# Kernel optimization log

Measured on AMD Instinct MI355X. Metric: run time of the kernel, lower is better.

## Reference

```python
import jax, jax.numpy as jnp
import numpy as np
from jax import lax

A_NUM = 2
N_LAYER = 4
DIM0 = 64   # fr_inner_dim_0 == signal_dim_0 (forced by view/squeeze logic)
DIM1 = 256  # fr_inner_dim_1
SD0 = 64
SD1 = 64
K_OUT = 8
UPS = 4
EPS = 1e-5
BSZ = 64


def setup_inputs() -> dict:
    key = jax.random.key(0)
    ks = jax.random.split(key, 16)
    s = 0.05
    f32 = jnp.float32
    inp = jax.random.normal(ks[0], (BSZ, 2, SD0, SD1), f32)
    # ComplexConv2d2 weights stored squeezed to their effective matmul form.
    W_in_r = jax.random.normal(ks[1], (DIM1 * A_NUM, SD1), f32) * s
    W_in_i = jax.random.normal(ks[2], (DIM1 * A_NUM, SD1), f32) * s
    W_pre_r = jax.random.normal(ks[3], (A_NUM,), f32) * s
    W_pre_i = jax.random.normal(ks[4], (A_NUM,), f32) * s
    Wm_r = jax.random.normal(ks[5], (2 * N_LAYER, SD0, SD0), f32) * s
    Wm_i = jax.random.normal(ks[6], (2 * N_LAYER, SD0, SD0), f32) * s
    Wc_r = jax.random.normal(ks[7], (N_LAYER, A_NUM), f32) * s
    Wc_i = jax.random.normal(ks[8], (N_LAYER, A_NUM), f32) * s
    W_l3_r = jax.random.normal(ks[9], (DIM0 * A_NUM, SD0), f32) * s
    W_l3_i = jax.random.normal(ks[10], (DIM0 * A_NUM, SD0), f32) * s
    conv1_w = jax.random.normal(ks[11], (N_LAYER, A_NUM, A_NUM, 3, 3), f32) * s
    conv2_w = jax.random.normal(ks[12], (N_LAYER, A_NUM, A_NUM, 3, 3), f32) * s
    bn1_g = jnp.ones((N_LAYER, A_NUM), f32)
    bn1_b = jnp.zeros((N_LAYER, A_NUM), f32)
    bn2_g = jnp.ones((N_LAYER, A_NUM), f32)
    bn2_b = jnp.zeros((N_LAYER, A_NUM), f32)
    W_out = jax.random.normal(ks[13], (A_NUM, 1, K_OUT, K_OUT), f32) * s
    return {"inp": inp, "W_in_r": W_in_r, "W_in_i": W_in_i, "W_pre_r": W_pre_r,
            "W_pre_i": W_pre_i, "Wm_r": Wm_r, "Wm_i": Wm_i, "Wc_r": Wc_r,
            "Wc_i": Wc_i, "W_l3_r": W_l3_r, "W_l3_i": W_l3_i,
            "conv1_w": conv1_w, "bn1_g": bn1_g, "bn1_b": bn1_b,
            "conv2_w": conv2_w, "bn2_g": bn2_g, "bn2_b": bn2_b, "W_out": W_out}


def _circ_conv(x, w):
    xp = jnp.pad(x, ((0, 0), (0, 0), (1, 1), (1, 1)), mode='wrap')
    return lax.conv_general_dilated(xp, w, (1, 1), 'VALID',
                                    dimension_numbers=('NCHW', 'OIHW', 'NCHW'))


def _bn(x, g, b):
    mu = jnp.mean(x, axis=(0, 2, 3), keepdims=True)
    var = jnp.var(x, axis=(0, 2, 3), keepdims=True)
    return (x - mu) * lax.rsqrt(var + EPS) * g[None, :, None, None] + b[None, :, None, None]


def _forward(inp, W_in_r, W_in_i, W_pre_r, W_pre_i, Wm_r, Wm_i, Wc_r, Wc_i,
             W_l3_r, W_l3_i, conv1_w, bn1_g, bn1_b, conv2_w, bn2_g, bn2_b, W_out):
    bsz = inp.shape[0]
    xr, xi = inp[:, 0], inp[:, 1]  # (b, sd0, sd1)
    # input_layer: complex conv, kernel (1, sd1) -> contraction over width
    yr = jnp.einsum('bhw,cw->bch', xr, W_in_r) - jnp.einsum('bhw,cw->bch', xi, W_in_i)
    yi = jnp.einsum('bhw,cw->bch', xi, W_in_r) + jnp.einsum('bhw,cw->bch', xr, W_in_i)
    xreal = yr.reshape(bsz, A_NUM, DIM1, DIM0).transpose(0, 1, 3, 2)  # (b,A,dim0,dim1)
    ximag = yi.reshape(bsz, A_NUM, DIM1, DIM0).transpose(0, 1, 3, 2)
    # concat_pre: complex 1x1 conv, A_NUM -> 1 channel
    x_real = (jnp.einsum('bahw,a->bhw', xreal, W_pre_r) - jnp.einsum('bahw,a->bhw', ximag, W_pre_i))[:, None]
    x_imag = (jnp.einsum('bahw,a->bhw', ximag, W_pre_r) + jnp.einsum('bahw,a->bhw', xreal, W_pre_i))[:, None]
    Gr, Gi = x_real, x_imag  # loop-invariant Gnk

    def phase_branch(xr_, xi_, Wr, Wi):
        a, c = xr_[:, 0], xi_[:, 0]  # (b, dim0, dim1)
        # complex conv kernel (sd0,1) == matmul over height
        Ir = (jnp.einsum('bhw,ch->bcw', a, Wr) - jnp.einsum('bhw,ch->bcw', c, Wi))[:, None]
        Ii = (jnp.einsum('bhw,ch->bcw', c, Wr) + jnp.einsum('bhw,ch->bcw', a, Wi))[:, None]
        s_ = 1.0 + jnp.log(Ir * Ir + Ii * Ii)
        EIr, EIi = s_ * Ir, -s_ * Ii
        ur, ui = Wr.T, Wi.T
        zr = jnp.einsum('hc,bncw->bnhw', ur, EIr) - jnp.einsum('hc,bncw->bnhw', ui, EIi)
        zi = jnp.einsum('hc,bncw->bnhw', ur, EIi) + jnp.einsum('hc,bncw->bnhw', ui, EIr)
        wr = jnp.sum(Gr * zr - Gi * zi, axis=3)  # (b,1,dim0)
        wi = jnp.sum(Gr * zi + Gi * zr, axis=3)
        ang = jnp.arctan2(wi, wr)[..., None]  # broadcast over dim1
        cr, ci = jnp.cos(ang), -jnp.sin(ang)
        return Gr * cr - Gi * ci, Gr * ci + Gi * cr

    for i in range(N_LAYER):
        x1r, x1i = phase_branch(x_real, x_imag, Wm_r[i], Wm_i[i])
        x2r, x2i = phase_branch(x_real, x_imag, Wm_r[i + N_LAYER], Wm_i[i + N_LAYER])
        sr = jnp.concatenate([x1r, x2r], 1)
        si = jnp.concatenate([x1i, x2i], 1)
        x_real = (jnp.einsum('bahw,a->bhw', sr, Wc_r[i]) - jnp.einsum('bahw,a->bhw', si, Wc_i[i]))[:, None]
        x_imag = (jnp.einsum('bahw,a->bhw', si, Wc_r[i]) + jnp.einsum('bahw,a->bhw', sr, Wc_i[i]))[:, None]

    # input_layer3: complex conv kernel (sd0,1), 1 -> dim0*A_NUM channels
    a, c = x_real[:, 0], x_imag[:, 0]
    fr = (jnp.einsum('bhw,ch->bcw', a, W_l3_r) - jnp.einsum('bhw,ch->bcw', c, W_l3_i)).reshape(bsz, -1)
    fi = (jnp.einsum('bhw,ch->bcw', c, W_l3_r) + jnp.einsum('bhw,ch->bcw', a, W_l3_i)).reshape(bsz, -1)
    m = jnp.max(jnp.sqrt(fr * fr + fi * fi), axis=1, keepdims=True)
    fr, fi = fr / m, fi / m
    fr = fr.reshape(bsz, A_NUM, DIM0, DIM1)
    fi = fi.reshape(bsz, A_NUM, DIM0, DIM1)
    x = jnp.sqrt(fr * fr + fi * fi)

    for i in range(N_LAYER):
        h = jax.nn.relu(_bn(_circ_conv(x, conv1_w[i]), bn1_g[i], bn1_b[i]))
        h = _bn(_circ_conv(h, conv2_w[i]), bn2_g[i], bn2_b[i])
        x = jax.nn.relu(x + h)

    # ConvTranspose2d(A_NUM, 1, K_OUT, stride=UPS, padding=2, output_padding=1)
    wt = jnp.flip(W_out, (2, 3)).transpose(1, 0, 2, 3)  # (1, A_NUM, k, k)
    pad_lo = K_OUT - 1 - 2
    pad_hi = pad_lo + 1
    y = lax.conv_general_dilated(x, wt, (1, 1),
                                 [(pad_lo, pad_hi), (pad_lo, pad_hi)],
                                 lhs_dilation=(UPS, UPS),
                                 dimension_numbers=('NCHW', 'OIHW', 'NCHW'))
    return y[:, 0]


def reference(inp, W_in_r, W_in_i, W_pre_r, W_pre_i, Wm_r, Wm_i, Wc_r, Wc_i,
              W_l3_r, W_l3_i, conv1_w, bn1_g, bn1_b, conv2_w, bn2_g, bn2_b, W_out):
    return _forward(inp, W_in_r, W_in_i, W_pre_r, W_pre_i, Wm_r, Wm_i, Wc_r, Wc_i,
                    W_l3_r, W_l3_i, conv1_w, bn1_g, bn1_b, conv2_w, bn2_g, bn2_b, W_out)
```

## Files before the change

### kernel.cpp

```cpp
#include <hip/hip_runtime.h>
#include <hip/hip_bf16.h>
#include <math.h>


__global__ void k0_prep(const float* __restrict__ Wr, const float* __restrict__ Wi,
                        const float* __restrict__ pr, const float* __restrict__ pi,
                        float* __restrict__ ArT, float* __restrict__ AiT,
                        float2* __restrict__ C) {
    int w  = blockIdx.x;
    int w2 = threadIdx.x;
    float p0r = pr[0], p1r = pr[1], p0i = pi[0], p1i = pi[1];
    float wr0 = Wr[w2 * 64 + w],         wi0 = Wi[w2 * 64 + w];
    float wr1 = Wr[(256 + w2) * 64 + w], wi1 = Wi[(256 + w2) * 64 + w];
    ArT[w * 256 + w2] = p0r * wr0 - p0i * wi0 + p1r * wr1 - p1i * wi1;
    AiT[w * 256 + w2] = p0r * wi0 + p0i * wr0 + p1r * wi1 + p1i * wr1;
    if (w2 < 64) C[w * 64 + w2] = make_float2(1.f, 0.f);
}

__global__ void k0b_T(const float* __restrict__ Wmr, const float* __restrict__ Wmi,
                      float* __restrict__ WmrT, float* __restrict__ WmiT) {
    int m = blockIdx.x;
    int t = threadIdx.x;
    const float* sr = Wmr + m * 4096;
    const float* si = Wmi + m * 4096;
    float* dr = WmrT + m * 4096;
    float* di = WmiT + m * 4096;
    for (int k = t; k < 4096; k += 256) {
        int c = k >> 6, h = k & 63;
        dr[h * 64 + c] = sr[k];
        di[h * 64 + c] = si[k];
    }
}

__global__ __launch_bounds__(256) void k1_G(const float* __restrict__ inp,
                                            const float* __restrict__ ArT,
                                            const float* __restrict__ AiT,
                                            float* __restrict__ Gr, float* __restrict__ Gi) {
    int hc = blockIdx.x;
    int b  = blockIdx.y;
    int t  = threadIdx.x;
    __shared__ float sxr[8][64], sxi[8][64];
    int base_r = (b * 2 + 0) * 4096 + hc * 8 * 64;
    int base_i = (b * 2 + 1) * 4096 + hc * 8 * 64;
    for (int k = t; k < 512; k += 256) {
        int r = k >> 6, w = k & 63;
        sxr[r][w] = inp[base_r + r * 64 + w];
        sxi[r][w] = inp[base_i + r * 64 + w];
    }
    __syncthreads();
    float accr[8], acci[8];
#pragma unroll
    for (int r = 0; r < 8; r++) { accr[r] = 0.f; acci[r] = 0.f; }
    for (int k = 0; k < 64; k++) {
        float ar = ArT[k * 256 + t], ai = AiT[k * 256 + t];
#pragma unroll
        for (int r = 0; r < 8; r++) {
            float xr = sxr[r][k], xi = sxi[r][k];
            accr[r] += xr * ar - xi * ai;
            acci[r] += xi * ar + xr * ai;
        }
    }
#pragma unroll
    for (int r = 0; r < 8; r++) {
        int h = hc * 8 + r;
        Gr[(b * 64 + h) * 256 + t] = accr[r];
        Gi[(b * 64 + h) * 256 + t] = acci[r];
    }
}

__global__ __launch_bounds__(512) void k2_layer(const float* __restrict__ Gr,
                                                const float* __restrict__ Gi,
                                                const float2* __restrict__ C,
                                                const float* __restrict__ Wmr,
                                                const float* __restrict__ Wmi,
                                                const float* __restrict__ WmrT,
                                                const float* __restrict__ WmiT,
                                                float2* __restrict__ wsum, int layer) {
    int wc = blockIdx.x;
    int b  = blockIdx.y;
    int t = threadIdx.x, tx = t & 63, ty = t >> 6;
    __shared__ float2 sX[4096];
    __shared__ float2 sE[4096];
    int h0 = __builtin_amdgcn_readfirstlane(ty << 3);

    int gbase = b * 16384 + wc * 64 + tx;
    float gr_[8], gi_[8];
#pragma unroll
    for (int r = 0; r < 8; r++) {
        int h = h0 + r;
        float gr = Gr[gbase + h * 256], gi = Gi[gbase + h * 256];
        gr_[r] = gr; gi_[r] = gi;
        float2 c = C[b * 64 + h];
        sX[h * 64 + tx] = make_float2(c.x * gr - c.y * gi, c.x * gi + c.y * gr);
    }
    __syncthreads();

    for (int j = 0; j < 2; j++) {
        int mat = layer + 4 * j;
        const float* Wr0  = Wmr  + mat * 4096 + h0 * 64;
        const float* Wi0  = Wmi  + mat * 4096 + h0 * 64;
        const float* WrT0 = WmrT + mat * 4096 + h0 * 64;
        const float* WiT0 = WmiT + mat * 4096 + h0 * 64;

        float Ir[8] = {0,0,0,0,0,0,0,0}, Ii[8] = {0,0,0,0,0,0,0,0};
#pragma unroll 4
        for (int h = 0; h < 64; h++) {
            float2 x = sX[h * 64 + tx];
#pragma unroll
            for (int r = 0; r < 8; r++) {
                float wr = Wr0[r * 64 + h], wi = Wi0[r * 64 + h];
                Ir[r] += wr * x.x - wi * x.y;
                Ii[r] += wr * x.y + wi * x.x;
            }
        }
#pragma unroll
        for (int r = 0; r < 8; r++) {
            float m2 = Ir[r] * Ir[r] + Ii[r] * Ii[r];
            float s = 1.f + __logf(m2);
            sE[(h0 + r) * 64 + tx] = make_float2(s * Ir[r], -s * Ii[r]);
        }
        __syncthreads();

        float Zr[8] = {0,0,0,0,0,0,0,0}, Zi[8] = {0,0,0,0,0,0,0,0};
#pragma unroll 4
        for (int c = 0; c < 64; c++) {
            float2 e = sE[c * 64 + tx];
#pragma unroll
            for (int r = 0; r < 8; r++) {
                float wr = WrT0[r * 64 + c], wi = WiT0[r * 64 + c];
                Zr[r] += wr * e.x - wi * e.y;
                Zi[r] += wr * e.y + wi * e.x;
            }
        }
#pragma unroll
        for (int r = 0; r < 8; r++) {
            int h = h0 + r;
            float pr = gr_[r] * Zr[r] - gi_[r] * Zi[r];
            float pi = gr_[r] * Zi[r] + gi_[r] * Zr[r];
#pragma unroll
            for (int off = 32; off > 0; off >>= 1) {
                pr += __shfl_xor(pr, off);
                pi += __shfl_xor(pi, off);
            }
            if (tx == 0) wsum[((b * 64 + h) * 2 + j) * 4 + wc] = make_float2(pr, pi);
        }
        __syncthreads();
    }
}

__global__ void k3_cupdate(const float2* __restrict__ wsum, float2* __restrict__ C,
                           const float* __restrict__ Wcr, const float* __restrict__ Wci,
                           int layer) {
    int id = blockIdx.x * 256 + threadIdx.x;
    float accr = 0.f, acci = 0.f;
#pragma unroll
    for (int j = 0; j < 2; j++) {
        float wr = 0.f, wi = 0.f;
#pragma unroll
        for (int wc = 0; wc < 4; wc++) {
            float2 p = wsum[(id * 2 + j) * 4 + wc];
            wr += p.x; wi += p.y;
        }
        float m2 = wr * wr + wi * wi;
        float cr, ci;
        if (m2 > 0.f) {
            float inv = 1.f / sqrtf(m2);
            cr = wr * inv; ci = -wi * inv;
        } else { cr = 1.f; ci = 0.f; }
        float wcr = Wcr[layer * 2 + j], wci = Wci[layer * 2 + j];
        accr += cr * wcr - ci * wci;
        acci += ci * wcr + cr * wci;
    }
    C[id] = make_float2(accr, acci);
}

__global__ __launch_bounds__(1024) void k4_proj(const float* __restrict__ Gr,
                                                const float* __restrict__ Gi,
                                                const float2* __restrict__ C,
                                                const float* __restrict__ W3r,
                                                const float* __restrict__ W3i,
                                                float* __restrict__ xmag,
                                                float* __restrict__ pmax) {
    int wc = blockIdx.x;
    int cb = blockIdx.y;
    int b  = blockIdx.z;
    int t = threadIdx.x, tx = t & 63, ty = t >> 6;
    __shared__ float2 sX[4096];
    int c0 = __builtin_amdgcn_readfirstlane(ty << 2);
    const float* W3r0 = W3r + (cb * 64 + c0) * 64;
    const float* W3i0 = W3i + (cb * 64 + c0) * 64;
    int gbase = b * 16384 + wc * 64 + tx;
#pragma unroll
    for (int r = 0; r < 4; r++) {
        int h = (ty << 2) + r;
        float gr = Gr[gbase + h * 256], gi = Gi[gbase + h * 256];
        float2 c = C[b * 64 + h];
        sX[h * 64 + tx] = make_float2(c.x * gr - c.y * gi, c.x * gi + c.y * gr);
    }
    __syncthreads();
    float Fr[4] = {0,0,0,0}, Fi[4] = {0,0,0,0};
#pragma unroll 8
    for (int h = 0; h < 64; h++) {
        float2 x = sX[h * 64 + tx];
#pragma unroll
        for (int r = 0; r < 4; r++) {
            float wr = W3r0[r * 64 + h], wi = W3i0[r * 64 + h];
            Fr[r] += wr * x.x - wi * x.y;
            Fi[r] += wr * x.y + wi * x.x;
        }
    }
    float mx = 0.f;
#pragma unroll
    for (int r = 0; r < 4; r++) {
        int cl = (ty << 2) + r;
        float mag = sqrtf(Fr[r] * Fr[r] + Fi[r] * Fi[r]);
        xmag[(b * 128 + cb * 64 + cl) * 256 + wc * 64 + tx] = mag;
        mx = fmaxf(mx, mag);
    }
#pragma unroll
    for (int off = 32; off > 0; off >>= 1) mx = fmaxf(mx, __shfl_xor(mx, off));
    __syncthreads();
    float* scratch = (float*)sX;
    if (tx == 0) scratch[ty] = mx;
    __syncthreads();
    if (t == 0) {
        float m = scratch[0];
#pragma unroll
        for (int k = 1; k < 16; k++) m = fmaxf(m, scratch[k]);
        pmax[b * 8 + cb * 4 + wc] = m;
    }
}

__global__ __launch_bounds__(256) void k_conv1f(const float* __restrict__ xin,
                                                const float* __restrict__ h2,
                                                const float* __restrict__ cw,
                                                const float* __restrict__ stats2,
                                                const float* __restrict__ pmax,
                                                float* __restrict__ hout,
                                                float* __restrict__ xout,
                                                float* __restrict__ psum,
                                                float* __restrict__ psumsq,
                                                int layer) {
    int hb = blockIdx.x;
    int co = blockIdx.y;
    int b  = blockIdx.z;
    int tx = threadIdx.x;
    float wgt[18];
    const float* wp = cw + layer * 36 + co * 18;
#pragma unroll
    for (int k = 0; k < 18; k++) wgt[k] = wp[k];
    float sc0 = 0.f, sc1 = 0.f, sh0 = 0.f, sh1 = 0.f, inv = 1.f;
    if (layer == 0) {
        float m = 0.f;
#pragma unroll
        for (int k = 0; k < 8; k++) m = fmaxf(m, pmax[b * 8 + k]);
        inv = 1.f / m;
    } else {
        sc0 = stats2[0]; sc1 = stats2[1]; sh0 = stats2[2]; sh1 = stats2[3];
    }
    int wm = (tx + 255) & 255, wpp = (tx + 1) & 255;
    float lsum = 0.f, lsq = 0.f;
    for (int r = 0; r < 4; r++) {
        int hh = hb * 4 + r;
        int hm = (hh + 63) & 63, hp = (hh + 1) & 63;
        const int rows[3] = {hm, hh, hp};
        const int cols[3] = {wm, tx, wpp};
        float acc = 0.f;
#pragma unroll
        for (int ci = 0; ci < 2; ci++) {
            const float* xp  = xin + (b * 2 + ci) * 16384;
            const float* hp2 = h2  + (b * 2 + ci) * 16384;
            float sc = ci ? sc1 : sc0, sh = ci ? sh1 : sh0;
            const float* wg = wgt + ci * 9;
#pragma unroll
            for (int kh = 0; kh < 3; kh++)
#pragma unroll
                for (int kw = 0; kw < 3; kw++) {
                    int idx = rows[kh] * 256 + cols[kw];
                    float v;
                    if (layer == 0) v = xp[idx] * inv;
                    else            v = fmaxf(xp[idx] + hp2[idx] * sc + sh, 0.f);
                    if (ci == co && kh == 1 && kw == 1)
                        xout[(b * 2 + co) * 16384 + hh * 256 + tx] = v;
                    acc += wg[kh * 3 + kw] * v;
                }
        }
        hout[((b * 2 + co) * 64 + hh) * 256 + tx] = acc;
        lsum += acc; lsq += acc * acc;
    }
#pragma unroll
    for (int off = 32; off > 0; off >>= 1) {
        lsum += __shfl_xor(lsum, off);
        lsq  += __shfl_xor(lsq, off);
    }
    __shared__ float ssum[4], ssq[4];
    int tyy = tx >> 6, lane = tx & 63;
    if (lane == 0) { ssum[tyy] = lsum; ssq[tyy] = lsq; }
    __syncthreads();
    if (tx == 0) {
        int bl = b * 16 + hb;
        psum[co * 1024 + bl]   = ssum[0] + ssum[1] + ssum[2] + ssum[3];
        psumsq[co * 1024 + bl] = ssq[0] + ssq[1] + ssq[2] + ssq[3];
    }
}

__global__ __launch_bounds__(256) void k_conv2(const float* __restrict__ h1,
                                               const float* __restrict__ cw,
                                               const float* __restrict__ stats1,
                                               float* __restrict__ hout,
                                               float* __restrict__ psum,
                                               float* __restrict__ psumsq,
                                               int layer) {
    int hb = blockIdx.x;
    int co = blockIdx.y;
    int b  = blockIdx.z;
    int tx = threadIdx.x;
    float wgt[18];
    const float* wp = cw + layer * 36 + co * 18;
#pragma unroll
    for (int k = 0; k < 18; k++) wgt[k] = wp[k];
    float sc0 = stats1[0], sc1 = stats1[1], sh0 = stats1[2], sh1 = stats1[3];
    int wm = (tx + 255) & 255, wpp = (tx + 1) & 255;
    float lsum = 0.f, lsq = 0.f;
    for (int r = 0; r < 4; r++) {
        int hh = hb * 4 + r;
        int hm = (hh + 63) & 63, hp = (hh + 1) & 63;
        const int rows[3] = {hm, hh, hp};
        const int cols[3] = {wm, tx, wpp};
        float acc = 0.f;
#pragma unroll
        for (int ci = 0; ci < 2; ci++) {
            const float* xp = h1 + (b * 2 + ci) * 16384;
            float sc = ci ? sc1 : sc0, sh = ci ? sh1 : sh0;
            const float* wg = wgt + ci * 9;
#pragma unroll
            for (int kh = 0; kh < 3; kh++)
#pragma unroll
                for (int kw = 0; kw < 3; kw++) {
                    float v = fmaxf(xp[rows[kh] * 256 + cols[kw]] * sc + sh, 0.f);
                    acc += wg[kh * 3 + kw] * v;
                }
        }
        hout[((b * 2 + co) * 64 + hh) * 256 + tx] = acc;
        lsum += acc; lsq += acc * acc;
    }
#pragma unroll
    for (int off = 32; off > 0; off >>= 1) {
        lsum += __shfl_xor(lsum, off);
        lsq  += __shfl_xor(lsq, off);
    }
    __shared__ float ssum[4], ssq[4];
    int tyy = tx >> 6, lane = tx & 63;
    if (lane == 0) { ssum[tyy] = lsum; ssq[tyy] = lsq; }
    __syncthreads();
    if (tx == 0) {
        int bl = b * 16 + hb;
        psum[co * 1024 + bl]   = ssum[0] + ssum[1] + ssum[2] + ssum[3];
        psumsq[co * 1024 + bl] = ssq[0] + ssq[1] + ssq[2] + ssq[3];
    }
}

__global__ void k_stats(const float* __restrict__ psum, const float* __restrict__ psumsq,
                        const float* __restrict__ g, const float* __restrict__ bb,
                        float* __restrict__ stats, int layer) {
    int ch = threadIdx.x >> 6, lane = threadIdx.x & 63;
    float s = 0.f, q = 0.f;
    for (int k = lane; k < 1024; k += 64) { s += psum[ch * 1024 + k]; q += psumsq[ch * 1024 + k]; }
#pragma unroll
    for (int off = 32; off > 0; off >>= 1) { s += __shfl_xor(s, off); q += __shfl_xor(q, off); }
    if (lane == 0) {
        const float N = 1048576.f;
        float mu = s / N;
        float var = q / N - mu * mu;
        float rs = rsqrtf(var + 1e-5f);
        float gamma = g[layer * 2 + ch];
        stats[ch]     = rs * gamma;
        stats[2 + ch] = bb[layer * 2 + ch] - mu * rs * gamma;
    }
}

__global__ void k9_out(const float* __restrict__ x3, const float* __restrict__ h2,
                       const float* __restrict__ stats2, const float* __restrict__ Wout,
                       float* __restrict__ out) {
    const int TOT = 64 * 257 * 1025;
    int id = blockIdx.x * 256 + threadIdx.x;
    if (id >= TOT) return;
    int b   = id / 263425;
    int rem = id - b * 263425;
    int oh  = rem / 1025;
    int ow  = rem - oh * 1025;
    int kh0 = (5 - oh) & 3;
    int kw0 = (5 - ow) & 3;
    float sc0 = stats2[0], sc1 = stats2[1], sh0 = stats2[2], sh1 = stats2[3];
    float acc = 0.f;
#pragma unroll
    for (int ah = 0; ah < 2; ah++) {
        int kh = kh0 + 4 * ah;
        int d = oh + kh - 5;
        if (d < 0 || d > 252) continue;
        int rh = d >> 2;
#pragma unroll
        for (int aw = 0; aw < 2; aw++) {
            int kw = kw0 + 4 * aw;
            int e = ow + kw - 5;
            if (e < 0 || e > 1020) continue;
            int rw = e >> 2;
#pragma unroll
            for (int ci = 0; ci < 2; ci++) {
                int idx = ((b * 2 + ci) * 64 + rh) * 256 + rw;
                float v = fmaxf(x3[idx] + h2[idx] * (ci ? sc1 : sc0) + (ci ? sh1 : sh0), 0.f);
                float wv = Wout[ci * 64 + (7 - kh) * 8 + (7 - kw)];
                acc += wv * v;
            }
        }
    }
    out[id] = acc;
}

extern "C" void kernel_launch(void* const* d_in, const int* in_sizes, int n_in,
                              void* d_out, int out_size, void* d_ws, size_t ws_size,
                              hipStream_t stream) {
    const float* inp   = (const float*)d_in[0];
    const float* Winr  = (const float*)d_in[1];
    const float* Wini  = (const float*)d_in[2];
    const float* Wprer = (const float*)d_in[3];
    const float* Wprei = (const float*)d_in[4];
    const float* Wmr   = (const float*)d_in[5];
    const float* Wmi   = (const float*)d_in[6];
    const float* Wcr   = (const float*)d_in[7];
    const float* Wci   = (const float*)d_in[8];
    const float* W3r   = (const float*)d_in[9];
    const float* W3i   = (const float*)d_in[10];
    const float* cw1   = (const float*)d_in[11];
    const float* bn1g  = (const float*)d_in[12];
    const float* bn1b  = (const float*)d_in[13];
    const float* cw2   = (const float*)d_in[14];
    const float* bn2g  = (const float*)d_in[15];
    const float* bn2b  = (const float*)d_in[16];
    const float* Wout  = (const float*)d_in[17];
    float* out = (float*)d_out;

    float* ws = (float*)d_ws;
    float*  ArT   = ws;
    float*  AiT   = ArT + 16384;
    float2* C     = (float2*)(AiT + 16384);
    float*  Gr    = (float*)C + 8192;
    float*  Gi    = Gr + 1048576;
    float2* wsum  = (float2*)(Gi + 1048576);
    float*  xmag  = (float*)wsum + 65536;
    float*  h2    = xmag + 2097152;
    float*  pmax  = h2 + 2097152;
    float*  psum1 = pmax + 512;
    float*  psq1  = psum1 + 2048;
    float*  psum2 = psq1 + 2048;
    float*  psq2  = psum2 + 2048;
    float*  stats = psq2 + 2048;
    float*  h1    = Gr;
    float*  WmrT  = h2;
    float*  WmiT  = h2 + 32768;
    float*  outS  = out;

    k0_prep<<<64, 256, 0, stream>>>(Winr, Wini, Wprer, Wprei, ArT, AiT, C);
    k0b_T<<<8, 256, 0, stream>>>(Wmr, Wmi, WmrT, WmiT);
    k1_G<<<dim3(8, 64), 256, 0, stream>>>(inp, ArT, AiT, Gr, Gi);
    for (int i = 0; i < 4; i++) {
        k2_layer<<<dim3(4, 64), 512, 0, stream>>>(Gr, Gi, C, Wmr, Wmi, WmrT, WmiT, wsum, i);
        k3_cupdate<<<16, 256, 0, stream>>>(wsum, C, Wcr, Wci, i);
    }
    k4_proj<<<dim3(4, 2, 64), 1024, 0, stream>>>(Gr, Gi, C, W3r, W3i, xmag, pmax);

    float* xbuf[5] = {xmag, outS, xmag, outS, xmag};
    for (int i = 0; i < 4; i++) {
        const float* xin = xbuf[i];
        float* xout = xbuf[i + 1];
        k_conv1f<<<dim3(16, 2, 64), 256, 0, stream>>>(xin, h2, cw1, stats + 4, pmax,
                                                      h1, xout, psum1, psq1, i);
        k_stats<<<1, 128, 0, stream>>>(psum1, psq1, bn1g, bn1b, stats, i);
        k_conv2<<<dim3(16, 2, 64), 256, 0, stream>>>(h1, cw2, stats, h2, psum2, psq2, i);
        k_stats<<<1, 128, 0, stream>>>(psum2, psq2, bn2g, bn2b, stats + 4, i);
    }
    k9_out<<<65857, 256, 0, stream>>>(xmag, h2, stats + 4, Wout, out);
}
```

Measured before the change: 667.8 us.

## Fold C-update and BN stats kernels into consumers; split k2 over j

The separate C-update kernel is removed. Each k2_layer block, and k4_proj, now rebuilds the per-batch coefficient vector in shared memory from the previous layer's wsum, using ping-pong wsum buffers. k2_layer is split across the two j matrices via the grid, which doubles the block count and reuses sX for the intermediate instead of a second shared buffer. The BN stats kernels are replaced by atomicAdd accumulation of channel sums, and each consumer derives scale and shift inline. This removes 12 small serialized launches, at the cost of redundant coefficient recomputation and order-dependent float atomics.

```diff
diff --git a/kernel.cpp b/kernel.cpp
--- a/kernel.cpp
+++ b/kernel.cpp
@@ -3,10 +3,12 @@
 #include <math.h>
 
 
+#define NPIX 1048576.f
+
 __global__ void k0_prep(const float* __restrict__ Wr, const float* __restrict__ Wi,
                         const float* __restrict__ pr, const float* __restrict__ pi,
                         float* __restrict__ ArT, float* __restrict__ AiT,
-                        float2* __restrict__ C) {
+                        float* __restrict__ accs) {
     int w  = blockIdx.x;
     int w2 = threadIdx.x;
     float p0r = pr[0], p1r = pr[1], p0i = pi[0], p1i = pi[1];
@@ -14,7 +16,7 @@
     float wr1 = Wr[(256 + w2) * 64 + w], wi1 = Wi[(256 + w2) * 64 + w];
     ArT[w * 256 + w2] = p0r * wr0 - p0i * wi0 + p1r * wr1 - p1i * wi1;
     AiT[w * 256 + w2] = p0r * wi0 + p0i * wr0 + p1r * wi1 + p1i * wr1;
-    if (w2 < 64) C[w * 64 + w2] = make_float2(1.f, 0.f);
+    if (w == 0 && w2 < 64) accs[w2] = 0.f;
 }
 
 __global__ void k0b_T(const float* __restrict__ Wmr, const float* __restrict__ Wmi,
@@ -70,18 +72,45 @@
 
 __global__ __launch_bounds__(512) void k2_layer(const float* __restrict__ Gr,
                                                 const float* __restrict__ Gi,
-                                                const float2* __restrict__ C,
+                                                const float2* __restrict__ wsumIn,
+                                                float2* __restrict__ wsumOut,
                                                 const float* __restrict__ Wmr,
                                                 const float* __restrict__ Wmi,
                                                 const float* __restrict__ WmrT,
                                                 const float* __restrict__ WmiT,
-                                                float2* __restrict__ wsum, int layer) {
+                                                const float* __restrict__ Wcr,
+                                                const float* __restrict__ Wci,
+                                                int layer) {
     int wc = blockIdx.x;
-    int b  = blockIdx.y;
-    int t = threadIdx.x, tx = t & 63, ty = t >> 6;
+    int j  = blockIdx.y;
+    int b  = blockIdx.z;
+    int t = threadIdx.x, tx = t & 63;
+    int h0 = __builtin_amdgcn_readfirstlane((t >> 6) << 3);
     __shared__ float2 sX[4096];
-    __shared__ float2 sE[4096];
-    int h0 = __builtin_amdgcn_readfirstlane(ty << 3);
+    __shared__ float2 sC[64];
+
+    if (layer == 0) {
+        if (t < 64) sC[t] = make_float2(1.f, 0.f);
+    } else if (t < 64) {
+        float accr = 0.f, acci = 0.f;
+#pragma unroll
+        for (int jj = 0; jj < 2; jj++) {
+            float wr = 0.f, wi = 0.f;
+#pragma unroll
+            for (int q = 0; q < 4; q++) {
+                float2 p = wsumIn[((b * 64 + t) * 2 + jj) * 4 + q];
+                wr += p.x; wi += p.y;
+            }
+            float m2 = wr * wr + wi * wi;
+            float cr = 1.f, ci = 0.f;
+            if (m2 > 0.f) { float inv = 1.f / sqrtf(m2); cr = wr * inv; ci = -wi * inv; }
+            float wcr = Wcr[(layer - 1) * 2 + jj], wci = Wci[(layer - 1) * 2 + jj];
+            accr += cr * wcr - ci * wci;
+            acci += ci * wcr + cr * wci;
+        }
+        sC[t] = make_float2(accr, acci);
+    }
+    __syncthreads();
 
     int gbase = b * 16384 + wc * 64 + tx;
     float gr_[8], gi_[8];
@@ -90,93 +119,67 @@
         int h = h0 + r;
         float gr = Gr[gbase + h * 256], gi = Gi[gbase + h * 256];
         gr_[r] = gr; gi_[r] = gi;
-        float2 c = C[b * 64 + h];
+        float2 c = sC[h];
         sX[h * 64 + tx] = make_float2(c.x * gr - c.y * gi, c.x * gi + c.y * gr);
     }
     __syncthreads();
 
-    for (int j = 0; j < 2; j++) {
-        int mat = layer + 4 * j;
-        const float* Wr0  = Wmr  + mat * 4096 + h0 * 64;
-        const float* Wi0  = Wmi  + mat * 4096 + h0 * 64;
-        const float* WrT0 = WmrT + mat * 4096 + h0 * 64;
-        const float* WiT0 = WmiT + mat * 4096 + h0 * 64;
-
-        float Ir[8] = {0,0,0,0,0,0,0,0}, Ii[8] = {0,0,0,0,0,0,0,0};
+    int mat = layer + 4 * j;
+    const float* Wr0  = Wmr  + mat * 4096 + h0 * 64;
+    const float* Wi0  = Wmi  + mat * 4096 + h0 * 64;
+    const float* WrT0 = WmrT + mat * 4096 + h0 * 64;
+    const float* WiT0 = WmiT + mat * 4096 + h0 * 64;
+
+    float Ir[8] = {0,0,0,0,0,0,0,0}, Ii[8] = {0,0,0,0,0,0,0,0};
 #pragma unroll 4
-        for (int h = 0; h < 64; h++) {
-            float2 x = sX[h * 64 + tx];
-#pragma unroll
-            for (int r = 0; r < 8; r++) {
-                float wr = Wr0[r * 64 + h], wi = Wi0[r * 64 + h];
-                Ir[r] += wr * x.x - wi * x.y;
-                Ii[r] += wr * x.y + wi * x.x;
-            }
-        }
+    for (int h = 0; h < 64; h++) {
+        float2 x = sX[h * 64 + tx];
 #pragma unroll
         for (int r = 0; r < 8; r++) {
-            float m2 = Ir[r] * Ir[r] + Ii[r] * Ii[r];
-            float s = 1.f + __logf(m2);
-            sE[(h0 + r) * 64 + tx] = make_float2(s * Ir[r], -s * Ii[r]);
-        }
-        __syncthreads();
-
-        float Zr[8] = {0,0,0,0,0,0,0,0}, Zi[8] = {0,0,0,0,0,0,0,0};
+            float wr = Wr0[r * 64 + h], wi = Wi0[r * 64 + h];
+            Ir[r] += wr * x.x - wi * x.y;
+            Ii[r] += wr * x.y + wi * x.x;
+        }
+    }
+    __syncthreads();
+#pragma unroll
+    for (int r = 0; r < 8; r++) {
+        float m2 = Ir[r] * Ir[r] + Ii[r] * Ii[r];
+        float s = 1.f + __logf(m2);
+        sX[(h0 + r) * 64 + tx] = make_float2(s * Ir[r], -s * Ii[r]);
+    }
+    __syncthreads();
+
+    float Zr[8] = {0,0,0,0,0,0,0,0}, Zi[8] = {0,0,0,0,0,0,0,0};
 #pragma unroll 4
-        for (int c = 0; c < 64; c++) {
-            float2 e = sE[c * 64 + tx];
-#pragma unroll
-            for (int r = 0; r < 8; r++) {
-                float wr = WrT0[r * 64 + c], wi = WiT0[r * 64 + c];
-                Zr[r] += wr * e.x - wi * e.y;
-                Zi[r] += wr * e.y + wi * e.x;
-            }
-        }
+    for (int c = 0; c < 64; c++) {
+        float2 e = sX[c * 64 + tx];
 #pragma unroll
         for (int r = 0; r < 8; r++) {
-            int h = h0 + r;
-            float pr = gr_[r] * Zr[r] - gi_[r] * Zi[r];
-            float pi = gr_[r] * Zi[r] + gi_[r] * Zr[r];
-#pragma unroll
-            for (int off = 32; off > 0; off >>= 1) {
-                pr += __shfl_xor(pr, off);
-                pi += __shfl_xor(pi, off);
-            }
-            if (tx == 0) wsum[((b * 64 + h) * 2 + j) * 4 + wc] = make_float2(pr, pi);
-        }
-        __syncthreads();
-    }
-}
-
-__global__ void k3_cupdate(const float2* __restrict__ wsum, float2* __restrict__ C,
-                           const float* __restrict__ Wcr, const float* __restrict__ Wci,
-                           int layer) {
-    int id = blockIdx.x * 256 + threadIdx.x;
-    float accr = 0.f, acci = 0.f;
-#pragma unroll
-    for (int j = 0; j < 2; j++) {
-        float wr = 0.f, wi = 0.f;
-#pragma unroll
-        for (int wc = 0; wc < 4; wc++) {
-            float2 p = wsum[(id * 2 + j) * 4 + wc];
-            wr += p.x; wi += p.y;
-        }
-        float m2 = wr * wr + wi * wi;
-        float cr, ci;
-        if (m2 > 0.f) {
-            float inv = 1.f / sqrtf(m2);
-            cr = wr * inv; ci = -wi * inv;
-        } else { cr = 1.f; ci = 0.f; }
-        float wcr = Wcr[layer * 2 + j], wci = Wci[layer * 2 + j];
-        accr += cr * wcr - ci * wci;
-        acci += ci * wcr + cr * wci;
-    }
-    C[id] = make_float2(accr, acci);
+            float wr = WrT0[r * 64 + c], wi = WiT0[r * 64 + c];
+            Zr[r] += wr * e.x - wi * e.y;
+            Zi[r] += wr * e.y + wi * e.x;
+        }
+    }
+#pragma unroll
+    for (int r = 0; r < 8; r++) {
+        int h = h0 + r;
+        float pr = gr_[r] * Zr[r] - gi_[r] * Zi[r];
+        float pi = gr_[r] * Zi[r] + gi_[r] * Zr[r];
+#pragma unroll
+        for (int off = 32; off > 0; off >>= 1) {
+            pr += __shfl_xor(pr, off);
+            pi += __shfl_xor(pi, off);
+        }
+        if (tx == 0) wsumOut[((b * 64 + h) * 2 + j) * 4 + wc] = make_float2(pr, pi);
+    }
 }
 
 __global__ __launch_bounds__(1024) void k4_proj(const float* __restrict__ Gr,
                                                 const float* __restrict__ Gi,
-                                                const float2* __restrict__ C,
+                                                const float2* __restrict__ wsumIn,
+                                                const float* __restrict__ Wcr,
+                                                const float* __restrict__ Wci,
                                                 const float* __restrict__ W3r,
                                                 const float* __restrict__ W3i,
                                                 float* __restrict__ xmag,
@@ -186,6 +189,27 @@
     int b  = blockIdx.z;
     int t = threadIdx.x, tx = t & 63, ty = t >> 6;
     __shared__ float2 sX[4096];
+    __shared__ float2 sC[64];
+    if (t < 64) {
+        float accr = 0.f, acci = 0.f;
+#pragma unroll
+        for (int jj = 0; jj < 2; jj++) {
+            float wr = 0.f, wi = 0.f;
+#pragma unroll
+            for (int q = 0; q < 4; q++) {
+                float2 p = wsumIn[((b * 64 + t) * 2 + jj) * 4 + q];
+                wr += p.x; wi += p.y;
+            }
+            float m2 = wr * wr + wi * wi;
+            float cr = 1.f, ci = 0.f;
+            if (m2 > 0.f) { float inv = 1.f / sqrtf(m2); cr = wr * inv; ci = -wi * inv; }
+            float wcr = Wcr[6 + jj], wci = Wci[6 + jj];
+            accr += cr * wcr - ci * wci;
+            acci += ci * wcr + cr * wci;
+        }
+        sC[t] = make_float2(accr, acci);
+    }
+    __syncthreads();
     int c0 = __builtin_amdgcn_readfirstlane(ty << 2);
     const float* W3r0 = W3r + (cb * 64 + c0) * 64;
     const float* W3i0 = W3i + (cb * 64 + c0) * 64;
@@ -194,7 +218,7 @@
     for (int r = 0; r < 4; r++) {
         int h = (ty << 2) + r;
         float gr = Gr[gbase + h * 256], gi = Gi[gbase + h * 256];
-        float2 c = C[b * 64 + h];
+        float2 c = sC[h];
         sX[h * 64 + tx] = make_float2(c.x * gr - c.y * gi, c.x * gi + c.y * gr);
     }
     __syncthreads();
@@ -234,12 +258,13 @@
 __global__ __launch_bounds__(256) void k_conv1f(const float* __restrict__ xin,
                                                 const float* __restrict__ h2,
                                                 const float* __restrict__ cw,
-                                                const float* __restrict__ stats2,
+                                                const float* __restrict__ bn2g,
+                                                const float* __restrict__ bn2b,
+                                                const float* __restrict__ accC2,
                                                 const float* __restrict__ pmax,
                                                 float* __restrict__ hout,
                                                 float* __restrict__ xout,
-                                                float* __restrict__ psum,
-                                                float* __restrict__ psumsq,
+                                                float* __restrict__ accC1,
                                                 int layer) {
     int hb = blockIdx.x;
     int co = blockIdx.y;
@@ -256,7 +281,14 @@
         for (int k = 0; k < 8; k++) m = fmaxf(m, pmax[b * 8 + k]);
         inv = 1.f / m;
     } else {
-        sc0 = stats2[0]; sc1 = stats2[1]; sh0 = stats2[2]; sh1 = stats2[3];
+        int pl = layer - 1;
+        float s0 = accC2[pl * 4 + 0], s1 = accC2[pl * 4 + 1];
+        float q0 = accC2[pl * 4 + 2], q1 = accC2[pl * 4 + 3];
+        float mu0 = s0 / NPIX, mu1 = s1 / NPIX;
+        float rs0 = rsqrtf(q0 / NPIX - mu0 * mu0 + 1e-5f);
+        float rs1 = rsqrtf(q1 / NPIX - mu1 * mu1 + 1e-5f);
+        sc0 = rs0 * bn2g[pl * 2 + 0]; sh0 = bn2b[pl * 2 + 0] - mu0 * sc0;
+        sc1 = rs1 * bn2g[pl * 2 + 1]; sh1 = bn2b[pl * 2 + 1] - mu1 * sc1;
     }
     int wm = (tx + 255) & 255, wpp = (tx + 1) & 255;
     float lsum = 0.f, lsq = 0.f;
@@ -298,18 +330,18 @@
     if (lane == 0) { ssum[tyy] = lsum; ssq[tyy] = lsq; }
     __syncthreads();
     if (tx == 0) {
-        int bl = b * 16 + hb;
-        psum[co * 1024 + bl]   = ssum[0] + ssum[1] + ssum[2] + ssum[3];
-        psumsq[co * 1024 + bl] = ssq[0] + ssq[1] + ssq[2] + ssq[3];
+        atomicAdd(&accC1[layer * 4 + co],     ssum[0] + ssum[1] + ssum[2] + ssum[3]);
+        atomicAdd(&accC1[layer * 4 + 2 + co], ssq[0] + ssq[1] + ssq[2] + ssq[3]);
     }
 }
 
 __global__ __launch_bounds__(256) void k_conv2(const float* __restrict__ h1,
                                                const float* __restrict__ cw,
-                                               const float* __restrict__ stats1,
+                                               const float* __restrict__ bn1g,
+                                               const float* __restrict__ bn1b,
+                                               const float* __restrict__ accC1,
                                                float* __restrict__ hout,
-                                               float* __restrict__ psum,
-                                               float* __restrict__ psumsq,
+                                               float* __restrict__ accC2,
                                                int layer) {
     int hb = blockIdx.x;
     int co = blockIdx.y;
@@ -319,7 +351,13 @@
     const float* wp = cw + layer * 36 + co * 18;
 #pragma unroll
     for (int k = 0; k < 18; k++) wgt[k] = wp[k];
-    float sc0 = stats1[0], sc1 = stats1[1], sh0 = stats1[2], sh1 = stats1[3];
+    float s0 = accC1[layer * 4 + 0], s1 = accC1[layer * 4 + 1];
+    float q0 = accC1[layer * 4 + 2], q1 = accC1[layer * 4 + 3];
+    float mu0 = s0 / NPIX, mu1 = s1 / NPIX;
+    float rs0 = rsqrtf(q0 / NPIX - mu0 * mu0 + 1e-5f);
+    float rs1 = rsqrtf(q1 / NPIX - mu1 * mu1 + 1e-5f);
+    float sc0 = rs0 * bn1g[layer * 2 + 0], sh0 = bn1b[layer * 2 + 0] - mu0 * sc0;
+    float sc1 = rs1 * bn1g[layer * 2 + 1], sh1 = bn1b[layer * 2 + 1] - mu1 * sc1;
     int wm = (tx + 255) & 255, wpp = (tx + 1) & 255;
     float lsum = 0.f, lsq = 0.f;
     for (int r = 0; r < 4; r++) {
@@ -354,44 +392,30 @@
     if (lane == 0) { ssum[tyy] = lsum; ssq[tyy] = lsq; }
     __syncthreads();
     if (tx == 0) {
-        int bl = b * 16 + hb;
-        psum[co * 1024 + bl]   = ssum[0] + ssum[1] + ssum[2] + ssum[3];
-        psumsq[co * 1024 + bl] = ssq[0] + ssq[1] + ssq[2] + ssq[3];
-    }
-}
-
-__global__ void k_stats(const float* __restrict__ psum, const float* __restrict__ psumsq,
-                        const float* __restrict__ g, const float* __restrict__ bb,
-                        float* __restrict__ stats, int layer) {
-    int ch = threadIdx.x >> 6, lane = threadIdx.x & 63;
-    float s = 0.f, q = 0.f;
-    for (int k = lane; k < 1024; k += 64) { s += psum[ch * 1024 + k]; q += psumsq[ch * 1024 + k]; }
-#pragma unroll
-    for (int off = 32; off > 0; off >>= 1) { s += __shfl_xor(s, off); q += __shfl_xor(q, off); }
-    if (lane == 0) {
-        const float N = 1048576.f;
-        float mu = s / N;
-        float var = q / N - mu * mu;
-        float rs = rsqrtf(var + 1e-5f);
-        float gamma = g[layer * 2 + ch];
-        stats[ch]     = rs * gamma;
-        stats[2 + ch] = bb[layer * 2 + ch] - mu * rs * gamma;
+        atomicAdd(&accC2[layer * 4 + co],     ssum[0] + ssum[1] + ssum[2] + ssum[3]);
+        atomicAdd(&accC2[layer * 4 + 2 + co], ssq[0] + ssq[1] + ssq[2] + ssq[3]);
     }
 }
 
 __global__ void k9_out(const float* __restrict__ x3, const float* __restrict__ h2,
-                       const float* __restrict__ stats2, const float* __restrict__ Wout,
-                       float* __restrict__ out) {
+                       const float* __restrict__ accC2,
+                       const float* __restrict__ bn2g, const float* __restrict__ bn2b,
+                       const float* __restrict__ Wout, float* __restrict__ out) {
     const int TOT = 64 * 257 * 1025;
     int id = blockIdx.x * 256 + threadIdx.x;
     if (id >= TOT) return;
+    float s0 = accC2[12], s1 = accC2[13], q0 = accC2[14], q1 = accC2[15];
+    float mu0 = s0 / NPIX, mu1 = s1 / NPIX;
+    float rs0 = rsqrtf(q0 / NPIX - mu0 * mu0 + 1e-5f);
+    float rs1 = rsqrtf(q1 / NPIX - mu1 * mu1 + 1e-5f);
+    float sc0 = rs0 * bn2g[6], sh0 = bn2b[6] - mu0 * sc0;
+    float sc1 = rs1 * bn2g[7], sh1 = bn2b[7] - mu1 * sc1;
     int b   = id / 263425;
     int rem = id - b * 263425;
     int oh  = rem / 1025;
     int ow  = rem - oh * 1025;
     int kh0 = (5 - oh) & 3;
     int kw0 = (5 - ow) & 3;
-    float sc0 = stats2[0], sc1 = stats2[1], sh0 = stats2[2], sh1 = stats2[3];
     float acc = 0.f;
 #pragma unroll
     for (int ah = 0; ah < 2; ah++) {
@@ -409,8 +433,7 @@
             for (int ci = 0; ci < 2; ci++) {
                 int idx = ((b * 2 + ci) * 64 + rh) * 256 + rw;
                 float v = fmaxf(x3[idx] + h2[idx] * (ci ? sc1 : sc0) + (ci ? sh1 : sh0), 0.f);
-                float wv = Wout[ci * 64 + (7 - kh) * 8 + (7 - kw)];
-                acc += wv * v;
+                acc += Wout[ci * 64 + (7 - kh) * 8 + (7 - kw)] * v;
             }
         }
     }
@@ -443,41 +466,36 @@
     float* ws = (float*)d_ws;
     float*  ArT   = ws;
     float*  AiT   = ArT + 16384;
-    float2* C     = (float2*)(AiT + 16384);
-    float*  Gr    = (float*)C + 8192;
+    float*  Gr    = AiT + 16384;
     float*  Gi    = Gr + 1048576;
-    float2* wsum  = (float2*)(Gi + 1048576);
-    float*  xmag  = (float*)wsum + 65536;
+    float2* wsum0 = (float2*)(Gi + 1048576);
+    float2* wsum1 = wsum0 + 32768;
+    float*  xmag  = (float*)(wsum1 + 32768);
     float*  h2    = xmag + 2097152;
     float*  pmax  = h2 + 2097152;
-    float*  psum1 = pmax + 512;
-    float*  psq1  = psum1 + 2048;
-    float*  psum2 = psq1 + 2048;
-    float*  psq2  = psum2 + 2048;
-    float*  stats = psq2 + 2048;
+    float*  accC1 = pmax + 512;
+    float*  accC2 = accC1 + 32;
     float*  h1    = Gr;
     float*  WmrT  = h2;
     float*  WmiT  = h2 + 32768;
     float*  outS  = out;
 
-    k0_prep<<<64, 256, 0, stream>>>(Winr, Wini, Wprer, Wprei, ArT, AiT, C);
+    k0_prep<<<64, 256, 0, stream>>>(Winr, Wini, Wprer, Wprei, ArT, AiT, accC1);
     k0b_T<<<8, 256, 0, stream>>>(Wmr, Wmi, WmrT, WmiT);
     k1_G<<<dim3(8, 64), 256, 0, stream>>>(inp, ArT, AiT, Gr, Gi);
+    float2* wsb[2] = {wsum0, wsum1};
     for (int i = 0; i < 4; i++) {
-        k2_layer<<<dim3(4, 64), 512, 0, stream>>>(Gr, Gi, C, Wmr, Wmi, WmrT, WmiT, wsum, i);
-        k3_cupdate<<<16, 256, 0, stream>>>(wsum, C, Wcr, Wci, i);
-    }
-    k4_proj<<<dim3(4, 2, 64), 1024, 0, stream>>>(Gr, Gi, C, W3r, W3i, xmag, pmax);
-
+        k2_layer<<<dim3(4, 2, 64), 512, 0, stream>>>(Gr, Gi, wsb[(i + 1) & 1], wsb[i & 1],
+                                                     Wmr, Wmi, WmrT, WmiT, Wcr, Wci, i);
+    }
+    k4_proj<<<dim3(4, 2, 64), 1024, 0, stream>>>(Gr, Gi, wsb[1], Wcr, Wci, W3r, W3i,
+                                                 xmag, pmax);
     float* xbuf[5] = {xmag, outS, xmag, outS, xmag};
     for (int i = 0; i < 4; i++) {
-        const float* xin = xbuf[i];
-        float* xout = xbuf[i + 1];
-        k_conv1f<<<dim3(16, 2, 64), 256, 0, stream>>>(xin, h2, cw1, stats + 4, pmax,
-                                                      h1, xout, psum1, psq1, i);
-        k_stats<<<1, 128, 0, stream>>>(psum1, psq1, bn1g, bn1b, stats, i);
-        k_conv2<<<dim3(16, 2, 64), 256, 0, stream>>>(h1, cw2, stats, h2, psum2, psq2, i);
-        k_stats<<<1, 128, 0, stream>>>(psum2, psq2, bn2g, bn2b, stats + 4, i);
-    }
-    k9_out<<<65857, 256, 0, stream>>>(xmag, h2, stats + 4, Wout, out);
-}
+        k_conv1f<<<dim3(16, 2, 64), 256, 0, stream>>>(xbuf[i], h2, cw1, bn2g, bn2b, accC2,
+                                                      pmax, h1, xbuf[i + 1], accC1, i);
+        k_conv2<<<dim3(16, 2, 64), 256, 0, stream>>>(h1, cw2, bn1g, bn1b, accC1, h2,
+                                                     accC2, i);
+    }
+    k9_out<<<65857, 256, 0, stream>>>(xmag, h2, accC2, bn2g, bn2b, Wout, out);
+}
```

Result: slower. 936.9 us (+40.3%).
